# Kernel tuning notes

Hardware: AMD Instinct MI355X
Metric: run time of the kernel (lower is better)

## Reference

```python
import jax, jax.numpy as jnp
import numpy as np

B, S, D, H = 2, 2048, 1024, 16
DK = D // H


def setup_inputs() -> dict:
    key = jax.random.key(0)
    ks = jax.random.split(key, 9)
    w_scale = 0.02  # small init for linear weights
    return {
        "query": jax.random.normal(ks[0], (B, S, D), jnp.float32),
        "key": jax.random.normal(ks[1], (B, S, D), jnp.float32),
        "value": jax.random.normal(ks[2], (B, S, D), jnp.float32),
        "mask": jax.random.randint(ks[3], (B, 1, S, S), 0, 2).astype(bool),
        "Wq": jax.random.normal(ks[4], (D, D), jnp.float32) * w_scale,
        "bq": jnp.zeros((D,), jnp.float32),
        "Wk": jax.random.normal(ks[5], (D, D), jnp.float32) * w_scale,
        "bk": jnp.zeros((D,), jnp.float32),
        "Wv": jax.random.normal(ks[6], (D, D), jnp.float32) * w_scale,
        "bv": jnp.zeros((D,), jnp.float32),
        "Wo": jax.random.normal(ks[7], (D, D), jnp.float32) * w_scale,
        "bo": jnp.zeros((D,), jnp.float32),
    }


def _split_heads(x):
    # [B,S,D] -> [B,H,S,DK]
    return x.reshape(B, S, H, DK).transpose(0, 2, 1, 3)


def reference(query, key, value, mask, Wq, bq, Wk, bk, Wv, bv, Wo, bo):
    Q = _split_heads(query @ Wq + bq)
    K = _split_heads(key @ Wk + bk)
    V = _split_heads(value @ Wv + bv)
    scores = jnp.einsum("bhqd,bhkd->bhqk", Q, K) / jnp.sqrt(jnp.float32(DK))
    scores = jnp.where(mask, -jnp.inf, scores)  # masked_fill(mask, -inf)
    attn_w = jax.nn.softmax(scores, axis=-1)
    attn_w = jnp.nan_to_num(attn_w, nan=0.0)  # rows fully masked -> 0
    out = jnp.einsum("bhqk,bhkd->bhqd", attn_w, V)
    out = out.transpose(0, 2, 1, 3).reshape(B, S, D)
    return out @ Wo + bo
```

## Files before the change

### kernel.cpp

```cpp
#include <hip/hip_runtime.h>
#include <hip/hip_bf16.h>
#include <cmath>
#include <cstdint>
#include <cstddef>

#define B_  2
#define S_  2048
#define D_  1024
#define H_  16
#define DK_ 64
#define NEG_BIG (-1e30f)

typedef __attribute__((ext_vector_type(8))) short bf16x8;
typedef __attribute__((ext_vector_type(4))) float f32x4;
typedef __attribute__((ext_vector_type(16))) float f32x16;

static __device__ __forceinline__ unsigned short f2bf(float f) {
  __hip_bfloat16 h = __float2bfloat16(f);
  return *reinterpret_cast<unsigned short*>(&h);
}

static __device__ __forceinline__ unsigned cvtpk(float lo, float hi) {
  unsigned d;
  asm("v_cvt_pk_bf16_f32 %0, %1, %2" : "=v"(d) : "v"(lo), "v"(hi));
  return d;
}
#define SWAP32(a, b) asm("v_permlane32_swap_b32 %0, %1" : "+v"(a), "+v"(b))

__global__ void pack_mask_kernel(const int* __restrict__ mask,
                                 unsigned* __restrict__ bits, int nwords) {
  int i = blockIdx.x * blockDim.x + threadIdx.x;
  if (i >= nwords) return;
  const int* p = mask + (size_t)i * 32;
  unsigned w = 0;
#pragma unroll
  for (int j = 0; j < 32; ++j) w |= (p[j] != 0 ? (1u << j) : 0u);
  bits[i] = w;
}

__global__ void cvt_f32_bf16_kernel(const float* __restrict__ q,
                                    const float* __restrict__ k,
                                    const float* __restrict__ v,
                                    unsigned short* __restrict__ qo,
                                    unsigned short* __restrict__ ko,
                                    unsigned short* __restrict__ vo, int n8) {
  int i = blockIdx.x * blockDim.x + threadIdx.x;
  if (i >= n8) return;
  const float* in = (blockIdx.y == 0) ? q : (blockIdx.y == 1) ? k : v;
  unsigned short* out = (blockIdx.y == 0) ? qo : (blockIdx.y == 1) ? ko : vo;
  const float4* p = reinterpret_cast<const float4*>(in) + (size_t)i * 2;
  float4 a = p[0], b = p[1];
  ushort4 o0 = {f2bf(a.x), f2bf(a.y), f2bf(a.z), f2bf(a.w)};
  ushort4 o1 = {f2bf(b.x), f2bf(b.y), f2bf(b.z), f2bf(b.w)};
  ushort4* o = reinterpret_cast<ushort4*>(out) + (size_t)i * 2;
  o[0] = o0;
  o[1] = o1;
}

__global__ __launch_bounds__(256) void transpose_w_kernel(
    const float* __restrict__ w0, const float* __restrict__ w1,
    const float* __restrict__ w2, const float* __restrict__ w3,
    unsigned short* __restrict__ t0, unsigned short* __restrict__ t1,
    unsigned short* __restrict__ t2, unsigned short* __restrict__ t3) {
  __shared__ unsigned short tile[32][33];
  const int z = blockIdx.z;
  const float* W = (z == 0) ? w0 : (z == 1) ? w1 : (z == 2) ? w2 : w3;
  unsigned short* Wt = (z == 0) ? t0 : (z == 1) ? t1 : (z == 2) ? t2 : t3;
  const int r0 = blockIdx.y * 32, c0 = blockIdx.x * 32;
  const int t = threadIdx.x;
  {
    const int r = t >> 3, c4 = (t & 7) * 4;
    float4 v = *reinterpret_cast<const float4*>(&W[(size_t)(r0 + r) * D_ + c0 + c4]);
    tile[c4 + 0][r] = f2bf(v.x);
    tile[c4 + 1][r] = f2bf(v.y);
    tile[c4 + 2][r] = f2bf(v.z);
    tile[c4 + 3][r] = f2bf(v.w);
  }
  __syncthreads();
  {
    const int n = t >> 3, k4 = (t & 7) * 4;
    ushort4 o = {tile[n][k4 + 0], tile[n][k4 + 1], tile[n][k4 + 2], tile[n][k4 + 3]};
    *reinterpret_cast<ushort4*>(&Wt[(size_t)(c0 + n) * D_ + r0 + k4]) = o;
  }
}

typedef __attribute__((address_space(3))) unsigned int lds_u32;
typedef __attribute__((address_space(1))) const unsigned int glb_u32;

__global__ __launch_bounds__(256) void qkv_gemm_kernel(
    const unsigned short* __restrict__ qb, const unsigned short* __restrict__ kb,
    const unsigned short* __restrict__ vb, const unsigned short* __restrict__ wtq,
    const unsigned short* __restrict__ wtk, const unsigned short* __restrict__ wtv,
    const float* __restrict__ bq, const float* __restrict__ bk,
    const float* __restrict__ bv, unsigned short* __restrict__ Qh,
    unsigned short* __restrict__ Kh, unsigned short* __restrict__ VT) {
  constexpr int K = D_;
  __shared__ __attribute__((aligned(16))) unsigned short as_[64 * 32];
  __shared__ __attribute__((aligned(16))) unsigned short bs_[64 * 32];
  const int z = blockIdx.z;
  const unsigned short* A = (z == 0) ? qb : (z == 1) ? kb : vb;
  const unsigned short* Wt = (z == 0) ? wtq : (z == 1) ? wtk : wtv;
  const float* bias = (z == 0) ? bq : (z == 1) ? bk : bv;

  const int bm = blockIdx.x * 64, bn = blockIdx.y * 64;
  const int t = threadIdx.x, wv = t >> 6, lane = t & 63;
  const int r = lane & 15, g = lane >> 4;
  const int wm = (wv >> 1) * 32, wn = (wv & 1) * 32;
  const int grow = 16 * wv + (lane >> 2);
  const int gcol = (lane & 3) * 8;

  lds_u32* asl = (lds_u32*)(as_ + 16 * wv * 32);
  lds_u32* bsl = (lds_u32*)(bs_ + 16 * wv * 32);

  f32x4 acc[2][2] = {};

  for (int k0 = 0; k0 < K; k0 += 32) {
    __syncthreads();
    __builtin_amdgcn_global_load_lds(
        (glb_u32*)&A[(size_t)(bm + grow) * K + k0 + gcol], asl, 16, 0, 0);
    __builtin_amdgcn_global_load_lds(
        (glb_u32*)&Wt[(size_t)(bn + grow) * K + k0 + gcol], bsl, 16, 0, 0);
    __syncthreads();

    bf16x8 a0 = *reinterpret_cast<const bf16x8*>(&as_[(wm + r) * 32 + 8 * g]);
    bf16x8 a1 = *reinterpret_cast<const bf16x8*>(&as_[(wm + 16 + r) * 32 + 8 * g]);
    bf16x8 b0 = *reinterpret_cast<const bf16x8*>(&bs_[(wn + r) * 32 + 8 * g]);
    bf16x8 b1 = *reinterpret_cast<const bf16x8*>(&bs_[(wn + 16 + r) * 32 + 8 * g]);
    acc[0][0] = __builtin_amdgcn_mfma_f32_16x16x32_bf16(a0, b0, acc[0][0], 0, 0, 0);
    acc[0][1] = __builtin_amdgcn_mfma_f32_16x16x32_bf16(a0, b1, acc[0][1], 0, 0, 0);
    acc[1][0] = __builtin_amdgcn_mfma_f32_16x16x32_bf16(a1, b0, acc[1][0], 0, 0, 0);
    acc[1][1] = __builtin_amdgcn_mfma_f32_16x16x32_bf16(a1, b1, acc[1][1], 0, 0, 0);
  }

#pragma unroll
  for (int mf = 0; mf < 2; ++mf)
#pragma unroll
    for (int nf = 0; nf < 2; ++nf)
#pragma unroll
      for (int reg = 0; reg < 4; ++reg) {
        const int row = bm + wm + 16 * mf + 4 * g + reg;
        const int col = bn + wn + 16 * nf + r;
        const float v = acc[mf][nf][reg] + bias[col];
        const int bb = row >> 11, s = row & (S_ - 1);
        const int h = col >> 6, dk = col & (DK_ - 1);
        if (z == 0)
          Qh[(((size_t)(bb * H_ + h)) * S_ + s) * DK_ + dk] = f2bf(v * 0.125f);
        else if (z == 1)
          Kh[(((size_t)(bb * H_ + h)) * S_ + s) * DK_ + dk] = f2bf(v);
        else
          VT[(((size_t)(bb * H_ + h)) * DK_ + dk) * S_ + s] = f2bf(v);
      }
}

__global__ __launch_bounds__(256) void out_gemm_kernel(
    const unsigned short* __restrict__ A, const unsigned short* __restrict__ Wt,
    const float* __restrict__ bias, float* __restrict__ Cout) {
  constexpr int K = D_;
  __shared__ __attribute__((aligned(16))) unsigned short as_[64 * 32];
  __shared__ __attribute__((aligned(16))) unsigned short bs_[64 * 32];
  const int bm = blockIdx.x * 64, bn = blockIdx.y * 64;
  const int t = threadIdx.x, wv = t >> 6, lane = t & 63;
  const int r = lane & 15, g = lane >> 4;
  const int wm = (wv >> 1) * 32, wn = (wv & 1) * 32;
  const int grow = 16 * wv + (lane >> 2);
  const int gcol = (lane & 3) * 8;

  lds_u32* asl = (lds_u32*)(as_ + 16 * wv * 32);
  lds_u32* bsl = (lds_u32*)(bs_ + 16 * wv * 32);

  f32x4 acc[2][2] = {};

  for (int k0 = 0; k0 < K; k0 += 32) {
    __syncthreads();
    __builtin_amdgcn_global_load_lds(
        (glb_u32*)&A[(size_t)(bm + grow) * K + k0 + gcol], asl, 16, 0, 0);
    __builtin_amdgcn_global_load_lds(
        (glb_u32*)&Wt[(size_t)(bn + grow) * K + k0 + gcol], bsl, 16, 0, 0);
    __syncthreads();

    bf16x8 a0 = *reinterpret_cast<const bf16x8*>(&as_[(wm + r) * 32 + 8 * g]);
    bf16x8 a1 = *reinterpret_cast<const bf16x8*>(&as_[(wm + 16 + r) * 32 + 8 * g]);
    bf16x8 b0 = *reinterpret_cast<const bf16x8*>(&bs_[(wn + r) * 32 + 8 * g]);
    bf16x8 b1 = *reinterpret_cast<const bf16x8*>(&bs_[(wn + 16 + r) * 32 + 8 * g]);
    acc[0][0] = __builtin_amdgcn_mfma_f32_16x16x32_bf16(a0, b0, acc[0][0], 0, 0, 0);
    acc[0][1] = __builtin_amdgcn_mfma_f32_16x16x32_bf16(a0, b1, acc[0][1], 0, 0, 0);
    acc[1][0] = __builtin_amdgcn_mfma_f32_16x16x32_bf16(a1, b0, acc[1][0], 0, 0, 0);
    acc[1][1] = __builtin_amdgcn_mfma_f32_16x16x32_bf16(a1, b1, acc[1][1], 0, 0, 0);
  }

#pragma unroll
  for (int mf = 0; mf < 2; ++mf)
#pragma unroll
    for (int nf = 0; nf < 2; ++nf)
#pragma unroll
      for (int reg = 0; reg < 4; ++reg) {
        const int row = bm + wm + 16 * mf + 4 * g + reg;
        const int col = bn + wn + 16 * nf + r;
        Cout[(size_t)row * D_ + col] = acc[mf][nf][reg] + bias[col];
      }
}

__global__ __launch_bounds__(256) void attn_mfma_kernel(
    const unsigned short* __restrict__ Qh, const unsigned short* __restrict__ Kh,
    const unsigned short* __restrict__ VT, const unsigned* __restrict__ mbits,
    unsigned short* __restrict__ ctx) {
  __shared__ float mlds[4][32];
  __shared__ float llds[4][32];
  __shared__ float olds[3][2][16][64];

  const int flat = blockIdx.x;
  const int bh = (flat & 7) * 4 + ((flat >> 3) & 3);
  const int qblk = flat >> 5;
  const int b = bh >> 4, h = bh & 15;
  const int kh = threadIdx.x >> 6, lane = threadIdx.x & 63;
  const int ql = lane & 31, hi = lane >> 5;
  const int qrow = qblk * 32 + ql;

  const unsigned short* Qrow = &Qh[((size_t)bh * S_ + qrow) * DK_];
  bf16x8 qf[4];
#pragma unroll
  for (int i = 0; i < 4; ++i)
    qf[i] = *(const bf16x8*)&Qrow[16 * i + 8 * hi];

  const unsigned short* Khead = &Kh[(size_t)bh * S_ * DK_];
  const unsigned short* Vhead = &VT[(size_t)bh * DK_ * S_];
  const unsigned* mrow = &mbits[((size_t)b * S_ + qrow) * (S_ / 32)];

  f32x16 o0 = {}, o1 = {};
  float m = NEG_BIG, l = 0.f;

  const int tbeg = kh * 16, tend = tbeg + 16;
  bf16x8 kf[4];
#pragma unroll
  for (int i = 0; i < 4; ++i)
    kf[i] = *(const bf16x8*)&Khead[(size_t)(tbeg * 32 + ql) * DK_ + 16 * i + 8 * hi];
  unsigned mw = mrow[tbeg];

  for (int tt = tbeg; tt < tend; ++tt) {
    f32x16 sc = {};
    __builtin_amdgcn_s_setprio(1);
#pragma unroll
    for (int i = 0; i < 4; ++i)
      sc = __builtin_amdgcn_mfma_f32_32x32x16_bf16(kf[i], qf[i], sc, 0, 0, 0);
    __builtin_amdgcn_s_setprio(0);

    const int tn = (tt + 1 < tend) ? tt + 1 : tt;
    bf16x8 kn[4];
#pragma unroll
    for (int i = 0; i < 4; ++i)
      kn[i] = *(const bf16x8*)&Khead[(size_t)(tn * 32 + ql) * DK_ + 16 * i + 8 * hi];
    const unsigned mwn = mrow[tn];

    bf16x8 vf[2][2];
#pragma unroll
    for (int kk = 0; kk < 2; ++kk)
#pragma unroll
      for (int db = 0; db < 2; ++db)
        vf[kk][db] = *(const bf16x8*)
            &Vhead[(size_t)(db * 32 + ql) * S_ + tt * 32 + kk * 16 + 8 * hi];

    const unsigned msh = mw >> (4 * hi);
#pragma unroll
    for (int reg = 0; reg < 16; ++reg) {
      const int creg = (reg & 3) + 8 * (reg >> 2);
      if ((msh >> creg) & 1u) sc[reg] = NEG_BIG;
    }

    float px = sc[0];
#pragma unroll
    for (int reg = 1; reg < 16; ++reg) px = fmaxf(px, sc[reg]);
    px = fmaxf(px, __shfl_xor(px, 32));

    if (!__all(px - m <= 8.f)) {
      const float mn = fmaxf(m, px);
      const float alpha = __expf(m - mn);
      m = mn;
      l *= alpha;
#pragma unroll
      for (int reg = 0; reg < 16; ++reg) { o0[reg] *= alpha; o1[reg] *= alpha; }
    }

    float rs = 0.f;
#pragma unroll
    for (int reg = 0; reg < 16; ++reg) {
      sc[reg] = __expf(sc[reg] - m);
      rs += sc[reg];
    }
    rs += __shfl_xor(rs, 32);
    l += rs;

    unsigned w0 = cvtpk(sc[0], sc[1]),   w2p = cvtpk(sc[4], sc[5]);
    unsigned w1 = cvtpk(sc[2], sc[3]),   w3p = cvtpk(sc[6], sc[7]);
    unsigned u0 = cvtpk(sc[8], sc[9]),   u2p = cvtpk(sc[12], sc[13]);
    unsigned u1 = cvtpk(sc[10], sc[11]), u3p = cvtpk(sc[14], sc[15]);
    SWAP32(w0, w2p);
    SWAP32(w1, w3p);
    SWAP32(u0, u2p);
    SWAP32(u1, u3p);
    union { unsigned u[4]; bf16x8 v; } pu0, pu1;
    pu0.u[0] = w0; pu0.u[1] = w1; pu0.u[2] = w2p; pu0.u[3] = w3p;
    pu1.u[0] = u0; pu1.u[1] = u1; pu1.u[2] = u2p; pu1.u[3] = u3p;

    __builtin_amdgcn_s_setprio(1);
    o0 = __builtin_amdgcn_mfma_f32_32x32x16_bf16(pu0.v, vf[0][0], o0, 0, 0, 0);
    o0 = __builtin_amdgcn_mfma_f32_32x32x16_bf16(pu1.v, vf[1][0], o0, 0, 0, 0);
    o1 = __builtin_amdgcn_mfma_f32_32x32x16_bf16(pu0.v, vf[0][1], o1, 0, 0, 0);
    o1 = __builtin_amdgcn_mfma_f32_32x32x16_bf16(pu1.v, vf[1][1], o1, 0, 0, 0);
    __builtin_amdgcn_s_setprio(0);

#pragma unroll
    for (int i = 0; i < 4; ++i) kf[i] = kn[i];
    mw = mwn;
  }

  if (lane < 32) {
    mlds[kh][ql] = m;
    llds[kh][ql] = l;
  }
  if (kh < 3) {
#pragma unroll
    for (int reg = 0; reg < 16; ++reg) {
      olds[kh][0][reg][lane] = o0[reg];
      olds[kh][1][reg][lane] = o1[reg];
    }
  }
  __syncthreads();
  if (kh == 3) {
#pragma unroll
    for (int reg = 0; reg < 16; ++reg) {
      const int crow = (reg & 3) + 8 * (reg >> 2) + 4 * hi;
      const float m0 = mlds[0][crow], m1 = mlds[1][crow];
      const float m2 = mlds[2][crow], m3 = mlds[3][crow];
      const float ms = fmaxf(fmaxf(m0, m1), fmaxf(m2, m3));
      const float f0 = __expf(m0 - ms), f1 = __expf(m1 - ms);
      const float f2 = __expf(m2 - ms), f3 = __expf(m3 - ms);
      const float ls = llds[0][crow] * f0 + llds[1][crow] * f1 +
                       llds[2][crow] * f2 + llds[3][crow] * f3;
      const float inv = (ms == NEG_BIG) ? 0.f : 1.f / ls;
      const float v0 = (olds[0][0][reg][lane] * f0 + olds[1][0][reg][lane] * f1 +
                        olds[2][0][reg][lane] * f2 + o0[reg] * f3) * inv;
      const float v1 = (olds[0][1][reg][lane] * f0 + olds[1][1][reg][lane] * f1 +
                        olds[2][1][reg][lane] * f2 + o1[reg] * f3) * inv;
      const int q = qblk * 32 + crow;
      unsigned short* cp = &ctx[((size_t)(b * S_ + q)) * D_ + h * DK_];
      cp[ql] = f2bf(v0);
      cp[32 + ql] = f2bf(v1);
    }
  }
}

extern "C" void kernel_launch(void* const* d_in, const int* in_sizes, int n_in,
                              void* d_out, int out_size, void* d_ws,
                              size_t ws_size, hipStream_t stream) {
  const float* query = (const float*)d_in[0];
  const float* key   = (const float*)d_in[1];
  const float* value = (const float*)d_in[2];
  const int*   mask  = (const int*)d_in[3];
  const float* Wq = (const float*)d_in[4];
  const float* bq = (const float*)d_in[5];
  const float* Wk = (const float*)d_in[6];
  const float* bk = (const float*)d_in[7];
  const float* Wv = (const float*)d_in[8];
  const float* bv = (const float*)d_in[9];
  const float* Wo = (const float*)d_in[10];
  const float* bo = (const float*)d_in[11];
  float* out = (float*)d_out;

  const size_t nElem = (size_t)B_ * S_ * D_;
  const size_t wElem = (size_t)D_ * D_;
  unsigned short* ws = (unsigned short*)d_ws;
  unsigned short* qb   = ws;
  unsigned short* kb   = qb + nElem;
  unsigned short* vb   = kb + nElem;
  unsigned short* wtq  = vb + nElem;
  unsigned short* wtk  = wtq + wElem;
  unsigned short* wtv  = wtk + wElem;
  unsigned short* wto  = wtv + wElem;
  unsigned short* Qh   = wto + wElem;
  unsigned short* Kh   = Qh + nElem;
  unsigned short* VT   = Kh + nElem;
  unsigned short* ctxb = VT + nElem;
  unsigned* mbits = (unsigned*)(ctxb + nElem);

  {
    const int nwords = B_ * S_ * S_ / 32;
    pack_mask_kernel<<<(nwords + 255) / 256, 256, 0, stream>>>(mask, mbits, nwords);
  }
  {
    const int n8 = (int)(nElem / 8);
    dim3 grid((n8 + 255) / 256, 3);
    cvt_f32_bf16_kernel<<<grid, 256, 0, stream>>>(query, key, value, qb, kb, vb, n8);
  }
  {
    dim3 grid(32, 32, 4);
    transpose_w_kernel<<<grid, 256, 0, stream>>>(Wq, Wk, Wv, Wo, wtq, wtk, wtv, wto);
  }
  {
    dim3 grid(64, 16, 3);
    qkv_gemm_kernel<<<grid, 256, 0, stream>>>(qb, kb, vb, wtq, wtk, wtv,
                                              bq, bk, bv, Qh, Kh, VT);
  }
  attn_mfma_kernel<<<2048, 256, 0, stream>>>(Qh, Kh, VT, mbits, ctxb);
  {
    dim3 grid(64, 16);
    out_gemm_kernel<<<grid, 256, 0, stream>>>(ctxb, wto, bo, out);
  }
}
```

Before: 360.4 us.

## Enlarge GEMM tiles, ballot-pack mask, exp2 softmax, restructure attention loop

Several independent changes land together. The QKV and output GEMMs move from 64x64 to 128x128 block tiles with a 4x4 MFMA fragment grid per wave, which raises data reuse per LDS load at the cost of more registers and fewer blocks. The mask packing now reads one element per thread and builds each word with a wavefront ballot, replacing 32 serial loads per thread. The attention inner loop is rewritten as a macro with double-buffered K fragments and pointer-increment addressing, drops the setprio hints, and folds log2(e) into the Q scale so exp2f can be used with a looser rescale threshold.

New measurement: 352.1 us. 2.3% less time.

```diff
diff --git a/kernel.cpp b/kernel.cpp
--- a/kernel.cpp
+++ b/kernel.cpp
@@ -10,6 +10,7 @@
 #define H_  16
 #define DK_ 64
 #define NEG_BIG (-1e30f)
+#define QSCALE 0.1803368801111204f
 
 typedef __attribute__((ext_vector_type(8))) short bf16x8;
 typedef __attribute__((ext_vector_type(4))) float f32x4;
@@ -27,15 +28,16 @@
 }
 #define SWAP32(a, b) asm("v_permlane32_swap_b32 %0, %1" : "+v"(a), "+v"(b))
 
+typedef __attribute__((address_space(3))) unsigned int lds_u32;
+typedef __attribute__((address_space(1))) const unsigned int glb_u32;
+
 __global__ void pack_mask_kernel(const int* __restrict__ mask,
-                                 unsigned* __restrict__ bits, int nwords) {
-  int i = blockIdx.x * blockDim.x + threadIdx.x;
-  if (i >= nwords) return;
-  const int* p = mask + (size_t)i * 32;
-  unsigned w = 0;
-#pragma unroll
-  for (int j = 0; j < 32; ++j) w |= (p[j] != 0 ? (1u << j) : 0u);
-  bits[i] = w;
+                                 unsigned* __restrict__ bits) {
+  const int t = blockIdx.x * 256 + threadIdx.x;
+  const unsigned long long ball = __ballot(mask[t] != 0);
+  const int lane = threadIdx.x & 63;
+  if ((lane & 31) == 0)
+    bits[t >> 5] = (lane == 0) ? (unsigned)ball : (unsigned)(ball >> 32);
 }
 
 __global__ void cvt_f32_bf16_kernel(const float* __restrict__ q,
@@ -84,9 +86,6 @@
   }
 }
 
-typedef __attribute__((address_space(3))) unsigned int lds_u32;
-typedef __attribute__((address_space(1))) const unsigned int glb_u32;
-
 __global__ __launch_bounds__(256) void qkv_gemm_kernel(
     const unsigned short* __restrict__ qb, const unsigned short* __restrict__ kb,
     const unsigned short* __restrict__ vb, const unsigned short* __restrict__ wtq,
@@ -95,56 +94,66 @@
     const float* __restrict__ bv, unsigned short* __restrict__ Qh,
     unsigned short* __restrict__ Kh, unsigned short* __restrict__ VT) {
   constexpr int K = D_;
-  __shared__ __attribute__((aligned(16))) unsigned short as_[64 * 32];
-  __shared__ __attribute__((aligned(16))) unsigned short bs_[64 * 32];
+  __shared__ __attribute__((aligned(16))) unsigned short as_[128 * 32];
+  __shared__ __attribute__((aligned(16))) unsigned short bs_[128 * 32];
   const int z = blockIdx.z;
   const unsigned short* A = (z == 0) ? qb : (z == 1) ? kb : vb;
   const unsigned short* Wt = (z == 0) ? wtq : (z == 1) ? wtk : wtv;
   const float* bias = (z == 0) ? bq : (z == 1) ? bk : bv;
 
-  const int bm = blockIdx.x * 64, bn = blockIdx.y * 64;
+  const int bm = blockIdx.x * 128, bn = blockIdx.y * 128;
   const int t = threadIdx.x, wv = t >> 6, lane = t & 63;
   const int r = lane & 15, g = lane >> 4;
-  const int wm = (wv >> 1) * 32, wn = (wv & 1) * 32;
-  const int grow = 16 * wv + (lane >> 2);
-  const int gcol = (lane & 3) * 8;
-
-  lds_u32* asl = (lds_u32*)(as_ + 16 * wv * 32);
-  lds_u32* bsl = (lds_u32*)(bs_ + 16 * wv * 32);
-
-  f32x4 acc[2][2] = {};
+  const int wr = (wv >> 1) * 64, wc = (wv & 1) * 64;
+  const int srow = 16 * wv + (lane >> 2);
+  const int scol = (lane & 3) * 8;
+
+  f32x4 acc[4][4] = {};
 
   for (int k0 = 0; k0 < K; k0 += 32) {
     __syncthreads();
     __builtin_amdgcn_global_load_lds(
-        (glb_u32*)&A[(size_t)(bm + grow) * K + k0 + gcol], asl, 16, 0, 0);
-    __builtin_amdgcn_global_load_lds(
-        (glb_u32*)&Wt[(size_t)(bn + grow) * K + k0 + gcol], bsl, 16, 0, 0);
+        (glb_u32*)&A[(size_t)(bm + srow) * K + k0 + scol],
+        (lds_u32*)(as_ + wv * 512), 16, 0, 0);
+    __builtin_amdgcn_global_load_lds(
+        (glb_u32*)&A[(size_t)(bm + 64 + srow) * K + k0 + scol],
+        (lds_u32*)(as_ + wv * 512 + 2048), 16, 0, 0);
+    __builtin_amdgcn_global_load_lds(
+        (glb_u32*)&Wt[(size_t)(bn + srow) * K + k0 + scol],
+        (lds_u32*)(bs_ + wv * 512), 16, 0, 0);
+    __builtin_amdgcn_global_load_lds(
+        (glb_u32*)&Wt[(size_t)(bn + 64 + srow) * K + k0 + scol],
+        (lds_u32*)(bs_ + wv * 512 + 2048), 16, 0, 0);
     __syncthreads();
 
-    bf16x8 a0 = *reinterpret_cast<const bf16x8*>(&as_[(wm + r) * 32 + 8 * g]);
-    bf16x8 a1 = *reinterpret_cast<const bf16x8*>(&as_[(wm + 16 + r) * 32 + 8 * g]);
-    bf16x8 b0 = *reinterpret_cast<const bf16x8*>(&bs_[(wn + r) * 32 + 8 * g]);
-    bf16x8 b1 = *reinterpret_cast<const bf16x8*>(&bs_[(wn + 16 + r) * 32 + 8 * g]);
-    acc[0][0] = __builtin_amdgcn_mfma_f32_16x16x32_bf16(a0, b0, acc[0][0], 0, 0, 0);
-    acc[0][1] = __builtin_amdgcn_mfma_f32_16x16x32_bf16(a0, b1, acc[0][1], 0, 0, 0);
-    acc[1][0] = __builtin_amdgcn_mfma_f32_16x16x32_bf16(a1, b0, acc[1][0], 0, 0, 0);
-    acc[1][1] = __builtin_amdgcn_mfma_f32_16x16x32_bf16(a1, b1, acc[1][1], 0, 0, 0);
-  }
-
-#pragma unroll
-  for (int mf = 0; mf < 2; ++mf)
-#pragma unroll
-    for (int nf = 0; nf < 2; ++nf)
+    bf16x8 a[4], bfr[4];
+#pragma unroll
+    for (int mf = 0; mf < 4; ++mf)
+      a[mf] = *reinterpret_cast<const bf16x8*>(&as_[(wr + 16 * mf + r) * 32 + 8 * g]);
+#pragma unroll
+    for (int nf = 0; nf < 4; ++nf)
+      bfr[nf] = *reinterpret_cast<const bf16x8*>(&bs_[(wc + 16 * nf + r) * 32 + 8 * g]);
+#pragma unroll
+    for (int mf = 0; mf < 4; ++mf)
+#pragma unroll
+      for (int nf = 0; nf < 4; ++nf)
+        acc[mf][nf] = __builtin_amdgcn_mfma_f32_16x16x32_bf16(a[mf], bfr[nf],
+                                                              acc[mf][nf], 0, 0, 0);
+  }
+
+#pragma unroll
+  for (int mf = 0; mf < 4; ++mf)
+#pragma unroll
+    for (int nf = 0; nf < 4; ++nf)
 #pragma unroll
       for (int reg = 0; reg < 4; ++reg) {
-        const int row = bm + wm + 16 * mf + 4 * g + reg;
-        const int col = bn + wn + 16 * nf + r;
+        const int row = bm + wr + 16 * mf + 4 * g + reg;
+        const int col = bn + wc + 16 * nf + r;
         const float v = acc[mf][nf][reg] + bias[col];
         const int bb = row >> 11, s = row & (S_ - 1);
         const int h = col >> 6, dk = col & (DK_ - 1);
         if (z == 0)
-          Qh[(((size_t)(bb * H_ + h)) * S_ + s) * DK_ + dk] = f2bf(v * 0.125f);
+          Qh[(((size_t)(bb * H_ + h)) * S_ + s) * DK_ + dk] = f2bf(v * QSCALE);
         else if (z == 1)
           Kh[(((size_t)(bb * H_ + h)) * S_ + s) * DK_ + dk] = f2bf(v);
         else
@@ -156,49 +165,136 @@
     const unsigned short* __restrict__ A, const unsigned short* __restrict__ Wt,
     const float* __restrict__ bias, float* __restrict__ Cout) {
   constexpr int K = D_;
-  __shared__ __attribute__((aligned(16))) unsigned short as_[64 * 32];
-  __shared__ __attribute__((aligned(16))) unsigned short bs_[64 * 32];
-  const int bm = blockIdx.x * 64, bn = blockIdx.y * 64;
+  __shared__ __attribute__((aligned(16))) unsigned short as_[128 * 32];
+  __shared__ __attribute__((aligned(16))) unsigned short bs_[128 * 32];
+  const int bm = blockIdx.x * 128, bn = blockIdx.y * 128;
   const int t = threadIdx.x, wv = t >> 6, lane = t & 63;
   const int r = lane & 15, g = lane >> 4;
-  const int wm = (wv >> 1) * 32, wn = (wv & 1) * 32;
-  const int grow = 16 * wv + (lane >> 2);
-  const int gcol = (lane & 3) * 8;
-
-  lds_u32* asl = (lds_u32*)(as_ + 16 * wv * 32);
-  lds_u32* bsl = (lds_u32*)(bs_ + 16 * wv * 32);
-
-  f32x4 acc[2][2] = {};
+  const int wr = (wv >> 1) * 64, wc = (wv & 1) * 64;
+  const int srow = 16 * wv + (lane >> 2);
+  const int scol = (lane & 3) * 8;
+
+  f32x4 acc[4][4] = {};
 
   for (int k0 = 0; k0 < K; k0 += 32) {
     __syncthreads();
     __builtin_amdgcn_global_load_lds(
-        (glb_u32*)&A[(size_t)(bm + grow) * K + k0 + gcol], asl, 16, 0, 0);
-    __builtin_amdgcn_global_load_lds(
-        (glb_u32*)&Wt[(size_t)(bn + grow) * K + k0 + gcol], bsl, 16, 0, 0);
+        (glb_u32*)&A[(size_t)(bm + srow) * K + k0 + scol],
+        (lds_u32*)(as_ + wv * 512), 16, 0, 0);
+    __builtin_amdgcn_global_load_lds(
+        (glb_u32*)&A[(size_t)(bm + 64 + srow) * K + k0 + scol],
+        (lds_u32*)(as_ + wv * 512 + 2048), 16, 0, 0);
+    __builtin_amdgcn_global_load_lds(
+        (glb_u32*)&Wt[(size_t)(bn + srow) * K + k0 + scol],
+        (lds_u32*)(bs_ + wv * 512), 16, 0, 0);
+    __builtin_amdgcn_global_load_lds(
+        (glb_u32*)&Wt[(size_t)(bn + 64 + srow) * K + k0 + scol],
+        (lds_u32*)(bs_ + wv * 512 + 2048), 16, 0, 0);
     __syncthreads();
 
-    bf16x8 a0 = *reinterpret_cast<const bf16x8*>(&as_[(wm + r) * 32 + 8 * g]);
-    bf16x8 a1 = *reinterpret_cast<const bf16x8*>(&as_[(wm + 16 + r) * 32 + 8 * g]);
-    bf16x8 b0 = *reinterpret_cast<const bf16x8*>(&bs_[(wn + r) * 32 + 8 * g]);
-    bf16x8 b1 = *reinterpret_cast<const bf16x8*>(&bs_[(wn + 16 + r) * 32 + 8 * g]);
-    acc[0][0] = __builtin_amdgcn_mfma_f32_16x16x32_bf16(a0, b0, acc[0][0], 0, 0, 0);
-    acc[0][1] = __builtin_amdgcn_mfma_f32_16x16x32_bf16(a0, b1, acc[0][1], 0, 0, 0);
-    acc[1][0] = __builtin_amdgcn_mfma_f32_16x16x32_bf16(a1, b0, acc[1][0], 0, 0, 0);
-    acc[1][1] = __builtin_amdgcn_mfma_f32_16x16x32_bf16(a1, b1, acc[1][1], 0, 0, 0);
-  }
-
-#pragma unroll
-  for (int mf = 0; mf < 2; ++mf)
-#pragma unroll
-    for (int nf = 0; nf < 2; ++nf)
+    bf16x8 a[4], bfr[4];
+#pragma unroll
+    for (int mf = 0; mf < 4; ++mf)
+      a[mf] = *reinterpret_cast<const bf16x8*>(&as_[(wr + 16 * mf + r) * 32 + 8 * g]);
+#pragma unroll
+    for (int nf = 0; nf < 4; ++nf)
+      bfr[nf] = *reinterpret_cast<const bf16x8*>(&bs_[(wc + 16 * nf + r) * 32 + 8 * g]);
+#pragma unroll
+    for (int mf = 0; mf < 4; ++mf)
+#pragma unroll
+      for (int nf = 0; nf < 4; ++nf)
+        acc[mf][nf] = __builtin_amdgcn_mfma_f32_16x16x32_bf16(a[mf], bfr[nf],
+                                                              acc[mf][nf], 0, 0, 0);
+  }
+
+#pragma unroll
+  for (int mf = 0; mf < 4; ++mf)
+#pragma unroll
+    for (int nf = 0; nf < 4; ++nf)
 #pragma unroll
       for (int reg = 0; reg < 4; ++reg) {
-        const int row = bm + wm + 16 * mf + 4 * g + reg;
-        const int col = bn + wn + 16 * nf + r;
+        const int row = bm + wr + 16 * mf + 4 * g + reg;
+        const int col = bn + wc + 16 * nf + r;
         Cout[(size_t)row * D_ + col] = acc[mf][nf][reg] + bias[col];
       }
 }
+
+#define ATTN_BODY(KF, KN, PRE)                                                 \
+  do {                                                                         \
+    const unsigned mw = *mp;                                                   \
+    ++mp;                                                                      \
+    const bf16x8 vf00 = *(const bf16x8*)(vb0);                                 \
+    const bf16x8 vf01 = *(const bf16x8*)(vb0 + 16);                            \
+    const bf16x8 vf10 = *(const bf16x8*)(vb1);                                 \
+    const bf16x8 vf11 = *(const bf16x8*)(vb1 + 16);                            \
+    vb0 += 32;                                                                 \
+    vb1 += 32;                                                                 \
+    if (PRE) {                                                                 \
+      KN[0] = *(const bf16x8*)(kbase);                                         \
+      KN[1] = *(const bf16x8*)(kbase + 16);                                    \
+      KN[2] = *(const bf16x8*)(kbase + 32);                                    \
+      KN[3] = *(const bf16x8*)(kbase + 48);                                    \
+      kbase += 2048;                                                           \
+    }                                                                          \
+    f32x16 sc = {};                                                            \
+    sc = __builtin_amdgcn_mfma_f32_32x32x16_bf16(KF[0], qf[0], sc, 0, 0, 0);   \
+    sc = __builtin_amdgcn_mfma_f32_32x32x16_bf16(KF[1], qf[1], sc, 0, 0, 0);   \
+    sc = __builtin_amdgcn_mfma_f32_32x32x16_bf16(KF[2], qf[2], sc, 0, 0, 0);   \
+    sc = __builtin_amdgcn_mfma_f32_32x32x16_bf16(KF[3], qf[3], sc, 0, 0, 0);   \
+    const unsigned msh = mw >> (4 * hi);                                       \
+    _Pragma("unroll") for (int reg = 0; reg < 16; ++reg) {                     \
+      const int creg = (reg & 3) + 8 * (reg >> 2);                             \
+      if ((msh >> creg) & 1u) sc[reg] = NEG_BIG;                               \
+    }                                                                          \
+    float px;                                                                  \
+    {                                                                          \
+      const float t0 = fmaxf(fmaxf(sc[0], sc[1]), sc[2]);                      \
+      const float t1 = fmaxf(fmaxf(sc[3], sc[4]), sc[5]);                      \
+      const float t2 = fmaxf(fmaxf(sc[6], sc[7]), sc[8]);                      \
+      const float t3 = fmaxf(fmaxf(sc[9], sc[10]), sc[11]);                    \
+      const float t4 = fmaxf(fmaxf(sc[12], sc[13]), sc[14]);                   \
+      const float u0 = fmaxf(fmaxf(t0, t1), t2);                               \
+      const float u1 = fmaxf(fmaxf(t3, t4), sc[15]);                           \
+      px = fmaxf(u0, u1);                                                      \
+    }                                                                          \
+    px = fmaxf(px, __shfl_xor(px, 32));                                        \
+    if (!__all(px - m <= 11.f)) {                                              \
+      const float mn = fmaxf(m, px);                                           \
+      const float al = exp2f(m - mn);                                          \
+      m = mn;                                                                  \
+      l *= al;                                                                 \
+      _Pragma("unroll") for (int reg = 0; reg < 16; ++reg) {                   \
+        o0[reg] *= al;                                                         \
+        o1[reg] *= al;                                                         \
+      }                                                                        \
+    }                                                                          \
+    _Pragma("unroll") for (int reg = 0; reg < 16; ++reg)                       \
+        sc[reg] = exp2f(sc[reg] - m);                                          \
+    {                                                                          \
+      const float s0 = (sc[0] + sc[1]) + (sc[2] + sc[3]);                      \
+      const float s1 = (sc[4] + sc[5]) + (sc[6] + sc[7]);                      \
+      const float s2 = (sc[8] + sc[9]) + (sc[10] + sc[11]);                    \
+      const float s3 = (sc[12] + sc[13]) + (sc[14] + sc[15]);                  \
+      float rs = (s0 + s1) + (s2 + s3);                                        \
+      rs += __shfl_xor(rs, 32);                                                \
+      l += rs;                                                                 \
+    }                                                                          \
+    unsigned w0 = cvtpk(sc[0], sc[1]), w2p = cvtpk(sc[4], sc[5]);              \
+    unsigned w1 = cvtpk(sc[2], sc[3]), w3p = cvtpk(sc[6], sc[7]);              \
+    unsigned u0 = cvtpk(sc[8], sc[9]), u2p = cvtpk(sc[12], sc[13]);            \
+    unsigned u1 = cvtpk(sc[10], sc[11]), u3p = cvtpk(sc[14], sc[15]);          \
+    SWAP32(w0, w2p);                                                           \
+    SWAP32(w1, w3p);                                                           \
+    SWAP32(u0, u2p);                                                           \
+    SWAP32(u1, u3p);                                                           \
+    union { unsigned u[4]; bf16x8 v; } pu0, pu1;                               \
+    pu0.u[0] = w0; pu0.u[1] = w1; pu0.u[2] = w2p; pu0.u[3] = w3p;              \
+    pu1.u[0] = u0; pu1.u[1] = u1; pu1.u[2] = u2p; pu1.u[3] = u3p;              \
+    o0 = __builtin_amdgcn_mfma_f32_32x32x16_bf16(pu0.v, vf00, o0, 0, 0, 0);    \
+    o0 = __builtin_amdgcn_mfma_f32_32x32x16_bf16(pu1.v, vf01, o0, 0, 0, 0);    \
+    o1 = __builtin_amdgcn_mfma_f32_32x32x16_bf16(pu0.v, vf10, o1, 0, 0, 0);    \
+    o1 = __builtin_amdgcn_mfma_f32_32x32x16_bf16(pu1.v, vf11, o1, 0, 0, 0);    \
+  } while (0)
 
 __global__ __launch_bounds__(256) void attn_mfma_kernel(
     const unsigned short* __restrict__ Qh, const unsigned short* __restrict__ Kh,
@@ -224,94 +320,30 @@
 
   const unsigned short* Khead = &Kh[(size_t)bh * S_ * DK_];
   const unsigned short* Vhead = &VT[(size_t)bh * DK_ * S_];
-  const unsigned* mrow = &mbits[((size_t)b * S_ + qrow) * (S_ / 32)];
 
   f32x16 o0 = {}, o1 = {};
   float m = NEG_BIG, l = 0.f;
 
-  const int tbeg = kh * 16, tend = tbeg + 16;
-  bf16x8 kf[4];
-#pragma unroll
-  for (int i = 0; i < 4; ++i)
-    kf[i] = *(const bf16x8*)&Khead[(size_t)(tbeg * 32 + ql) * DK_ + 16 * i + 8 * hi];
-  unsigned mw = mrow[tbeg];
-
-  for (int tt = tbeg; tt < tend; ++tt) {
-    f32x16 sc = {};
-    __builtin_amdgcn_s_setprio(1);
-#pragma unroll
-    for (int i = 0; i < 4; ++i)
-      sc = __builtin_amdgcn_mfma_f32_32x32x16_bf16(kf[i], qf[i], sc, 0, 0, 0);
-    __builtin_amdgcn_s_setprio(0);
-
-    const int tn = (tt + 1 < tend) ? tt + 1 : tt;
-    bf16x8 kn[4];
-#pragma unroll
-    for (int i = 0; i < 4; ++i)
-      kn[i] = *(const bf16x8*)&Khead[(size_t)(tn * 32 + ql) * DK_ + 16 * i + 8 * hi];
-    const unsigned mwn = mrow[tn];
-
-    bf16x8 vf[2][2];
-#pragma unroll
-    for (int kk = 0; kk < 2; ++kk)
-#pragma unroll
-      for (int db = 0; db < 2; ++db)
-        vf[kk][db] = *(const bf16x8*)
-            &Vhead[(size_t)(db * 32 + ql) * S_ + tt * 32 + kk * 16 + 8 * hi];
-
-    const unsigned msh = mw >> (4 * hi);
-#pragma unroll
-    for (int reg = 0; reg < 16; ++reg) {
-      const int creg = (reg & 3) + 8 * (reg >> 2);
-      if ((msh >> creg) & 1u) sc[reg] = NEG_BIG;
-    }
-
-    float px = sc[0];
-#pragma unroll
-    for (int reg = 1; reg < 16; ++reg) px = fmaxf(px, sc[reg]);
-    px = fmaxf(px, __shfl_xor(px, 32));
-
-    if (!__all(px - m <= 8.f)) {
-      const float mn = fmaxf(m, px);
-      const float alpha = __expf(m - mn);
-      m = mn;
-      l *= alpha;
-#pragma unroll
-      for (int reg = 0; reg < 16; ++reg) { o0[reg] *= alpha; o1[reg] *= alpha; }
-    }
-
-    float rs = 0.f;
-#pragma unroll
-    for (int reg = 0; reg < 16; ++reg) {
-      sc[reg] = __expf(sc[reg] - m);
-      rs += sc[reg];
-    }
-    rs += __shfl_xor(rs, 32);
-    l += rs;
-
-    unsigned w0 = cvtpk(sc[0], sc[1]),   w2p = cvtpk(sc[4], sc[5]);
-    unsigned w1 = cvtpk(sc[2], sc[3]),   w3p = cvtpk(sc[6], sc[7]);
-    unsigned u0 = cvtpk(sc[8], sc[9]),   u2p = cvtpk(sc[12], sc[13]);
-    unsigned u1 = cvtpk(sc[10], sc[11]), u3p = cvtpk(sc[14], sc[15]);
-    SWAP32(w0, w2p);
-    SWAP32(w1, w3p);
-    SWAP32(u0, u2p);
-    SWAP32(u1, u3p);
-    union { unsigned u[4]; bf16x8 v; } pu0, pu1;
-    pu0.u[0] = w0; pu0.u[1] = w1; pu0.u[2] = w2p; pu0.u[3] = w3p;
-    pu1.u[0] = u0; pu1.u[1] = u1; pu1.u[2] = u2p; pu1.u[3] = u3p;
-
-    __builtin_amdgcn_s_setprio(1);
-    o0 = __builtin_amdgcn_mfma_f32_32x32x16_bf16(pu0.v, vf[0][0], o0, 0, 0, 0);
-    o0 = __builtin_amdgcn_mfma_f32_32x32x16_bf16(pu1.v, vf[1][0], o0, 0, 0, 0);
-    o1 = __builtin_amdgcn_mfma_f32_32x32x16_bf16(pu0.v, vf[0][1], o1, 0, 0, 0);
-    o1 = __builtin_amdgcn_mfma_f32_32x32x16_bf16(pu1.v, vf[1][1], o1, 0, 0, 0);
-    __builtin_amdgcn_s_setprio(0);
-
-#pragma unroll
-    for (int i = 0; i < 4; ++i) kf[i] = kn[i];
-    mw = mwn;
-  }
+  const int tbeg = kh * 16;
+  const unsigned short* kbase = Khead + ((size_t)(tbeg * 32 + ql)) * DK_ + 8 * hi;
+  const unsigned short* vb0 = Vhead + (size_t)ql * S_ + tbeg * 32 + 8 * hi;
+  const unsigned short* vb1 = vb0 + (size_t)32 * S_;
+  const unsigned* mp = &mbits[((size_t)b * S_ + qrow) * (S_ / 32) + tbeg];
+
+  bf16x8 kfA[4], kfB[4];
+  kfA[0] = *(const bf16x8*)(kbase);
+  kfA[1] = *(const bf16x8*)(kbase + 16);
+  kfA[2] = *(const bf16x8*)(kbase + 32);
+  kfA[3] = *(const bf16x8*)(kbase + 48);
+  kbase += 2048;
+
+#pragma unroll 1
+  for (int it = 0; it < 7; ++it) {
+    ATTN_BODY(kfA, kfB, 1);
+    ATTN_BODY(kfB, kfA, 1);
+  }
+  ATTN_BODY(kfA, kfB, 1);
+  ATTN_BODY(kfB, kfA, 0);
 
   if (lane < 32) {
     mlds[kh][ql] = m;
@@ -332,8 +364,8 @@
       const float m0 = mlds[0][crow], m1 = mlds[1][crow];
       const float m2 = mlds[2][crow], m3 = mlds[3][crow];
       const float ms = fmaxf(fmaxf(m0, m1), fmaxf(m2, m3));
-      const float f0 = __expf(m0 - ms), f1 = __expf(m1 - ms);
-      const float f2 = __expf(m2 - ms), f3 = __expf(m3 - ms);
+      const float f0 = exp2f(m0 - ms), f1 = exp2f(m1 - ms);
+      const float f2 = exp2f(m2 - ms), f3 = exp2f(m3 - ms);
       const float ls = llds[0][crow] * f0 + llds[1][crow] * f1 +
                        llds[2][crow] * f2 + llds[3][crow] * f3;
       const float inv = (ms == NEG_BIG) ? 0.f : 1.f / ls;
@@ -382,10 +414,7 @@
   unsigned short* ctxb = VT + nElem;
   unsigned* mbits = (unsigned*)(ctxb + nElem);
 
-  {
-    const int nwords = B_ * S_ * S_ / 32;
-    pack_mask_kernel<<<(nwords + 255) / 256, 256, 0, stream>>>(mask, mbits, nwords);
-  }
+  pack_mask_kernel<<<(B_ * S_ * S_) / 256, 256, 0, stream>>>(mask, mbits);
   {
     const int n8 = (int)(nElem / 8);
     dim3 grid((n8 + 255) / 256, 3);
@@ -396,13 +425,13 @@
     transpose_w_kernel<<<grid, 256, 0, stream>>>(Wq, Wk, Wv, Wo, wtq, wtk, wtv, wto);
   }
   {
-    dim3 grid(64, 16, 3);
+    dim3 grid(32, 8, 3);
     qkv_gemm_kernel<<<grid, 256, 0, stream>>>(qb, kb, vb, wtq, wtk, wtv,
                                               bq, bk, bv, Qh, Kh, VT);
   }
   attn_mfma_kernel<<<2048, 256, 0, stream>>>(Qh, Kh, VT, mbits, ctxb);
   {
-    dim3 grid(64, 16);
+    dim3 grid(32, 8);
     out_gemm_kernel<<<grid, 256, 0, stream>>>(ctxb, wto, bo, out);
   }
 }
```
